# Performance work log

Measured on AMD Instinct MI355X. Metric: run time of the kernel, lower is better.

The kernel has to match this reference:

```python
import jax, jax.numpy as jnp
import numpy as np
from jax import lax

N = 1_000_000
H = 1024
POOL = 8
NF = 16
NS = 50
K = 5
PAD = (K - 1) // 2
D_IN = 3 + NF + NS  # 69
EPS = 1e-4


def setup_inputs() -> dict:
    key = jax.random.key(0)
    ks = jax.random.split(key, 14)
    def dense(k, fan_in, fan_out):
        lim = 1.0 / np.sqrt(fan_in)
        kw, kb = jax.random.split(k)
        w = jax.random.uniform(kw, (fan_in, fan_out), jnp.float32, -lim, lim)
        b = jax.random.uniform(kb, (fan_out,), jnp.float32, -lim, lim)
        return w, b
    x = jax.random.uniform(ks[0], (N, 2), jnp.float32)
    s = jax.random.normal(ks[1], (N, 1), jnp.float32)
    sse = jax.random.normal(ks[2], (N, NS), jnp.float32)
    sdf = jax.random.normal(ks[3], (1, 2, H, H), jnp.float32)
    lim_c = 1.0 / np.sqrt(2 * K * K)
    conv_w = jax.random.uniform(ks[4], (NF, 2, K, K), jnp.float32, -lim_c, lim_c)
    conv_b = jax.random.uniform(ks[5], (NF,), jnp.float32, -lim_c, lim_c)
    w1, b1 = dense(ks[6], D_IN, 128)
    w2, b2 = dense(ks[7], 128, 128)
    w3, b3 = dense(ks[8], 128, 96)
    w4, b4 = dense(ks[9], 96, 1)
    return {"x": x, "s": s, "sse": sse, "sdf": sdf,
            "conv_w": conv_w, "conv_b": conv_b,
            "w1": w1, "b1": b1, "w2": w2, "b2": b2,
            "w3": w3, "b3": b3, "w4": w4, "b4": b4}


def tensor_interp2d(A, pts, dx):
    # A: [C, Hh, Ww] feature map; pts: [N, 2] coords in [0,1] -> returns [N, C]
    C, Hh, Ww = A.shape
    gx = jnp.clip(pts[:, 0], dx, 1.0 - dx) * (Ww - 1)
    gy = jnp.clip(pts[:, 1], dx, 1.0 - dx) * (Hh - 1)
    x0 = jnp.floor(gx).astype(jnp.int32)
    y0 = jnp.floor(gy).astype(jnp.int32)
    x1 = jnp.minimum(x0 + 1, Ww - 1)
    y1 = jnp.minimum(y0 + 1, Hh - 1)
    wx = (gx - x0)[None, :]  # [1, N]
    wy = (gy - y0)[None, :]
    f00 = A[:, y0, x0]  # [C, N]
    f10 = A[:, y0, x1]
    f01 = A[:, y1, x0]
    f11 = A[:, y1, x1]
    out = (f00 * (1 - wx) * (1 - wy) + f10 * wx * (1 - wy)
           + f01 * (1 - wx) * wy + f11 * wx * wy)
    return out.T  # [N, C]


def reference(x, s, sse, sdf, conv_w, conv_b, w1, b1, w2, b2, w3, b3, w4, b4):
    # AvgPool2d(8, stride=8): exact reshape-mean since stride == kernel
    B, Cin, Hh, Ww = sdf.shape
    pooled = sdf.reshape(B, Cin, Hh // POOL, POOL, Ww // POOL, POOL).mean(axis=(3, 5))
    feat = lax.conv_general_dilated(pooled, conv_w, (1, 1), [(PAD, PAD), (PAD, PAD)],
                                    dimension_numbers=("NCHW", "OIHW", "NCHW"))
    feat = feat + conv_b[None, :, None, None]
    A = feat[0]  # squeeze -> [NF, 128, 128]
    x1 = tensor_interp2d(A, x, EPS)  # [N, NF]
    h = jnp.concatenate((x, s, sse, x1), axis=1)  # [N, 69]
    h = jax.nn.relu(h @ w1 + b1)
    h = jax.nn.relu(h @ w2 + b2)
    h = jax.nn.relu(h @ w3 + b3)
    return h @ w4 + b4  # [N, 1]
```

## Files before the change

kernel.cpp:

```cpp
#include <hip/hip_runtime.h>

#define EPS_ 1e-4f

typedef _Float16 f16;
typedef _Float16 f16x8 __attribute__((ext_vector_type(8)));
typedef _Float16 f16x4 __attribute__((ext_vector_type(4)));
typedef _Float16 f16x2 __attribute__((ext_vector_type(2)));
typedef __fp16 h16x2 __attribute__((ext_vector_type(2)));
typedef float f32x4v __attribute__((ext_vector_type(4)));
typedef float f32x2v __attribute__((ext_vector_type(2)));
typedef unsigned int u32;

__device__ inline f32x4v mfma16(f16x8 a, f16x8 b, f32x4v c) {
    return __builtin_amdgcn_mfma_f32_16x16x32_f16(a, b, c, 0, 0, 0);
}
__device__ inline f16x2 pk2(float a, float b) {
    h16x2 r = __builtin_amdgcn_cvt_pkrtz(a, b);
    return __builtin_bit_cast(f16x2, r);
}
__device__ inline u32 bc32(f16x2 v) { return __builtin_bit_cast(u32, v); }

__device__ inline f16x8 zero8() {
    f16x8 r;
#pragma unroll
    for (int i = 0; i < 8; i++) r[i] = (f16)0.f;
    return r;
}

__device__ inline f16x8 cvt8x2(f32x2v a, f32x2v b, f32x2v c, f32x2v d) {
    f16x2 p0 = pk2(a.x, a.y), p1 = pk2(b.x, b.y), p2 = pk2(c.x, c.y), p3 = pk2(d.x, d.y);
    f16x8 r;
    r[0] = p0[0]; r[1] = p0[1]; r[2] = p1[0]; r[3] = p1[1];
    r[4] = p2[0]; r[5] = p2[1]; r[6] = p3[0]; r[7] = p3[1];
    return r;
}

__global__ void pool_kernel(const float* __restrict__ sdf, float* __restrict__ pooled) {
    int t = blockIdx.x * blockDim.x + threadIdx.x;
    int c = t >> 14;
    int rem = t & 16383;
    int R = rem >> 7;
    int C = rem & 127;
    const float* base = sdf + c * 1048576 + (R * 8) * 1024 + C * 8;
    float sum = 0.f;
#pragma unroll
    for (int r = 0; r < 8; r++) {
        const float4* p = (const float4*)(base + r * 1024);
        float4 a = p[0];
        float4 b = p[1];
        sum += a.x + a.y + a.z + a.w + b.x + b.y + b.z + b.w;
    }
    pooled[t] = sum * (1.f / 64.f);
}

__global__ void conv_kernel(const float* __restrict__ pooled,
                            const float* __restrict__ conv_w,
                            const float* __restrict__ conv_b,
                            float* __restrict__ A) {
    int t = blockIdx.x * blockDim.x + threadIdx.x;
    int y = t >> 7, x = t & 127;
    float acc[16];
#pragma unroll
    for (int f = 0; f < 16; f++) acc[f] = conv_b[f];
#pragma unroll
    for (int c = 0; c < 2; c++) {
#pragma unroll
        for (int ky = 0; ky < 5; ky++) {
            int yy = y + ky - 2;
            if (yy < 0 || yy > 127) continue;
#pragma unroll
            for (int kx = 0; kx < 5; kx++) {
                int xx = x + kx - 2;
                if (xx < 0 || xx > 127) continue;
                float v = pooled[c * 16384 + yy * 128 + xx];
                int wbase = c * 25 + ky * 5 + kx;
#pragma unroll
                for (int f = 0; f < 16; f++)
                    acc[f] = fmaf(v, conv_w[f * 50 + wbase], acc[f]);
            }
        }
    }
    float4* out4 = (float4*)(A + t * 16);
#pragma unroll
    for (int q = 0; q < 4; q++)
        out4[q] = make_float4(acc[4 * q], acc[4 * q + 1], acc[4 * q + 2], acc[4 * q + 3]);
}

__global__ void pack_kernel(const float* __restrict__ w1, const float* __restrict__ b1,
                            const float* __restrict__ w2, const float* __restrict__ w3,
                            f16* __restrict__ frags) {
    int t = blockIdx.x * blockDim.x + threadIdx.x;
    if (t >= 80 * 64) return;
    int f = t >> 6, lane = t & 63;
    int g = lane >> 4, col = lane & 15;
    f16 v[8];
    if (f < 24) {
        int mf = f / 3, kc = f % 3;
        int o = mf * 16 + col;
#pragma unroll
        for (int i = 0; i < 8; i++) {
            int k = kc * 32 + g * 8 + i;
            float val = 0.f;
            if (k < 50) val = w1[(3 + k) * 128 + o];
            else if (k == 50) val = w1[0 * 128 + o];
            else if (k == 51) val = w1[1 * 128 + o];
            else if (k == 52) val = w1[2 * 128 + o];
            else if (k >= 56 && k < 72) val = w1[(53 + (k - 56)) * 128 + o];
            else if (k == 72) val = b1[o];
            v[i] = (f16)val;
        }
    } else if (f < 56) {
        int ff = f - 24, mf = ff >> 2, kc = ff & 3;
        int o = mf * 16 + col;
#pragma unroll
        for (int i = 0; i < 8; i++) {
            int k = kc * 32 + g * 8 + i;
            v[i] = (f16)w2[k * 128 + o];
        }
    } else {
        int ff = f - 56, mf = ff >> 2, kc = ff & 3;
        int o = mf * 16 + col;
#pragma unroll
        for (int i = 0; i < 8; i++) {
            int k = kc * 32 + g * 8 + i;
            v[i] = (f16)w3[k * 96 + o];
        }
    }
    f16* dst = frags + (f * 64 + lane) * 8;
#pragma unroll
    for (int i = 0; i < 8; i++) dst[i] = v[i];
}

__global__ void __launch_bounds__(768, 3) mlp_kernel(
    const float* __restrict__ x, const float* __restrict__ s,
    const float* __restrict__ sse, const float* __restrict__ Amat,
    const float4* __restrict__ fragsv,
    const float* __restrict__ b2, const float* __restrict__ b3,
    const float* __restrict__ w4, const float* __restrict__ b4,
    float* __restrict__ out) {
    __shared__ f16 wlds[40960];
    __shared__ f16 acth[12][2048];
    __shared__ float bias2[128];
    __shared__ float bias3[96];
    __shared__ float w4l[96];

    const int tid = threadIdx.x;
    const int wv = tid >> 6;
    const int lane = tid & 63;
    const int g = lane >> 4, col = lane & 15;
    const int swz = (col & 7) << 3;

    {
        float4* wl4 = (float4*)wlds;
        for (int i = tid; i < 5120; i += 768) wl4[i] = fragsv[i];
        if (tid < 128) bias2[tid] = b2[tid];
        if (tid < 96) { bias3[tid] = b3[tid]; w4l[tid] = w4[tid]; }
    }
    __syncthreads();
    const float b4v = b4[0];

    f16* ah = acth[wv];
    u32* ibA = (u32*)ah;
    u32* ibB = (u32*)ah + 192;

    const int wtotal = 31250;
    int wg = blockIdx.x * 12 + wv;
    const int wstride = gridDim.x * 12;

    f32x2v Axv, Bxv;

    auto INTERP = [&](f32x2v xv, u32* ib) {
        float gx = fminf(fmaxf(xv.x, EPS_), 1.f - EPS_) * 127.f;
        float gy = fminf(fmaxf(xv.y, EPS_), 1.f - EPS_) * 127.f;
        float fx0 = floorf(gx), fy0 = floorf(gy);
        int ix0 = (int)fx0, iy0 = (int)fy0;
        int ix1 = min(ix0 + 1, 127), iy1 = min(iy0 + 1, 127);
        float wx = gx - fx0, wy = gy - fy0;
        const f32x4v* A4 = (const f32x4v*)Amat;
        f32x4v f00 = A4[(iy0 * 128 + ix0) * 4 + g];
        f32x4v f10 = A4[(iy0 * 128 + ix1) * 4 + g];
        f32x4v f01 = A4[(iy1 * 128 + ix0) * 4 + g];
        f32x4v f11 = A4[(iy1 * 128 + ix1) * 4 + g];
        float w00 = (1.f - wx) * (1.f - wy), w10 = wx * (1.f - wy);
        float w01 = (1.f - wx) * wy, w11 = wx * wy;
        f32x4v r = f00 * w00 + f10 * w10 + f01 * w01 + f11 * w11;
        uint2 uv;
        uv.x = bc32(pk2(r.x, r.y));
        uv.y = bc32(pk2(r.z, r.w));
        *(uint2*)(ib + col * 12 + 2 * g) = uv;
    };

    auto LOADBUILD = [&](int pt0, f32x2v xv, const u32* ib, f16x8* bf) {
        const float* base = sse + (long)(pt0 + col) * 50;
        f32x2v c0[4];
#pragma unroll
        for (int q = 0; q < 4; q++) c0[q] = *(const f32x2v*)(base + 8 * g + 2 * q);
        bf[0] = cvt8x2(c0[0], c0[1], c0[2], c0[3]);
        if (g < 2) {
            f32x2v c1[4];
#pragma unroll
            for (int q = 0; q < 4; q++) c1[q] = *(const f32x2v*)(base + 32 + 8 * g + 2 * q);
            bf[1] = cvt8x2(c1[0], c1[1], c1[2], c1[3]);
        } else if (g == 2) {
            f32x2v e = *(const f32x2v*)(base + 48);
            float sv = s[pt0 + col];
            f16x8 t = zero8();
            t[0] = (f16)e.x; t[1] = (f16)e.y;
            t[2] = (f16)xv.x; t[3] = (f16)xv.y;
            t[4] = (f16)sv;
            bf[1] = t;
        } else {
            bf[1] = *(const f16x8*)(ib + col * 12);
        }
        if (g == 0) {
            bf[2] = *(const f16x8*)(ib + col * 12 + 4);
        } else if (g == 1) {
            f16x8 t = zero8();
            t[0] = (f16)1.f;
            bf[2] = t;
        } else {
            bf[2] = zero8();
        }
    };

    auto TRANS = [&](f32x4v* acc, const float* bias, f16x8* hbf) {
#pragma unroll
        for (int mf = 0; mf < 8; mf++) {
            f32x4v v = acc[mf];
            if (bias) {
                f32x4v bb = *(const f32x4v*)&bias[mf * 16 + g * 4];
                v = v + bb;
            }
            uint2 uv;
            uv.x = bc32(pk2(fmaxf(v.x, 0.f), fmaxf(v.y, 0.f)));
            uv.y = bc32(pk2(fmaxf(v.z, 0.f), fmaxf(v.w, 0.f)));
            *(uint2*)&ah[(col * 128 + mf * 16 + g * 4) ^ swz] = uv;
        }
#pragma unroll
        for (int kc = 0; kc < 4; kc++)
            hbf[kc] = *(const f16x8*)&ah[(col * 128 + kc * 32 + g * 8) ^ swz];
    };

    auto L4OUT = [&](f32x4v* acc3, int pt0) {
        float partial = 0.f;
#pragma unroll
        for (int mf = 0; mf < 6; mf++) {
            f32x4v bb = *(const f32x4v*)&bias3[mf * 16 + g * 4];
            f32x4v wv4 = *(const f32x4v*)&w4l[mf * 16 + g * 4];
            partial += fmaxf(acc3[mf].x + bb.x, 0.f) * wv4.x;
            partial += fmaxf(acc3[mf].y + bb.y, 0.f) * wv4.y;
            partial += fmaxf(acc3[mf].z + bb.z, 0.f) * wv4.z;
            partial += fmaxf(acc3[mf].w + bb.w, 0.f) * wv4.w;
        }
        partial += __shfl_xor(partial, 16);
        partial += __shfl_xor(partial, 32);
        if (g == 0) out[pt0 + col] = partial + b4v;
    };

    if (wg < wtotal) {
        Axv = *(const f32x2v*)(x + 2 * (wg * 32 + col));
        Bxv = *(const f32x2v*)(x + 2 * (wg * 32 + 16 + col));
    }

    for (; wg < wtotal; wg += wstride) {
        const int pt0 = wg * 32;

        INTERP(Axv, ibA);
        INTERP(Bxv, ibB);

        f16x8 bfA[3], bfB[3];
        LOADBUILD(pt0, Axv, ibA, bfA);
        LOADBUILD(pt0 + 16, Bxv, ibB, bfB);

        int wgn = wg + wstride;
        if (wgn < wtotal) {
            Axv = *(const f32x2v*)(x + 2 * (wgn * 32 + col));
            Bxv = *(const f32x2v*)(x + 2 * (wgn * 32 + 16 + col));
        }

        f32x4v accA[8], accB[8];
#pragma unroll
        for (int mf = 0; mf < 8; mf++) {
            accA[mf] = (f32x4v)(0.f);
            accB[mf] = (f32x4v)(0.f);
        }
#pragma unroll
        for (int kc = 0; kc < 3; kc++) {
#pragma unroll
            for (int mf = 0; mf < 8; mf++) {
                f16x8 wf = *(const f16x8*)&wlds[((mf * 3 + kc) * 64 + lane) * 8];
                accA[mf] = mfma16(wf, bfA[kc], accA[mf]);
                accB[mf] = mfma16(wf, bfB[kc], accB[mf]);
            }
        }

        f16x8 hbfA[4], hbfB[4];
        TRANS(accA, nullptr, hbfA);
        TRANS(accB, nullptr, hbfB);

        f32x4v acc2A[8], acc2B[8];
#pragma unroll
        for (int mf = 0; mf < 8; mf++) {
            acc2A[mf] = (f32x4v)(0.f);
            acc2B[mf] = (f32x4v)(0.f);
        }
#pragma unroll
        for (int kc = 0; kc < 4; kc++) {
#pragma unroll
            for (int mf = 0; mf < 8; mf++) {
                f16x8 wf = *(const f16x8*)&wlds[((24 + mf * 4 + kc) * 64 + lane) * 8];
                acc2A[mf] = mfma16(wf, hbfA[kc], acc2A[mf]);
                acc2B[mf] = mfma16(wf, hbfB[kc], acc2B[mf]);
            }
        }

        TRANS(acc2A, bias2, hbfA);
        TRANS(acc2B, bias2, hbfB);

        f32x4v acc3A[6], acc3B[6];
#pragma unroll
        for (int mf = 0; mf < 6; mf++) {
            acc3A[mf] = (f32x4v)(0.f);
            acc3B[mf] = (f32x4v)(0.f);
        }
#pragma unroll
        for (int kc = 0; kc < 4; kc++) {
#pragma unroll
            for (int mf = 0; mf < 6; mf++) {
                f16x8 wf = *(const f16x8*)&wlds[((56 + mf * 4 + kc) * 64 + lane) * 8];
                acc3A[mf] = mfma16(wf, hbfA[kc], acc3A[mf]);
                acc3B[mf] = mfma16(wf, hbfB[kc], acc3B[mf]);
            }
        }

        L4OUT(acc3A, pt0);
        L4OUT(acc3B, pt0 + 16);
    }
}

extern "C" void kernel_launch(void* const* d_in, const int* in_sizes, int n_in,
                              void* d_out, int out_size, void* d_ws, size_t ws_size,
                              hipStream_t stream) {
    const float* x      = (const float*)d_in[0];
    const float* s      = (const float*)d_in[1];
    const float* sse    = (const float*)d_in[2];
    const float* sdf    = (const float*)d_in[3];
    const float* conv_w = (const float*)d_in[4];
    const float* conv_b = (const float*)d_in[5];
    const float* w1     = (const float*)d_in[6];
    const float* b1     = (const float*)d_in[7];
    const float* w2     = (const float*)d_in[8];
    const float* b2     = (const float*)d_in[9];
    const float* w3     = (const float*)d_in[10];
    const float* b3     = (const float*)d_in[11];
    const float* w4     = (const float*)d_in[12];
    const float* b4     = (const float*)d_in[13];
    float* out = (float*)d_out;

    float* pooled = (float*)d_ws;
    float* A      = pooled + 32768;
    f16*   frags  = (f16*)d_ws;

    pool_kernel<<<128, 256, 0, stream>>>(sdf, pooled);
    conv_kernel<<<64, 256, 0, stream>>>(pooled, conv_w, conv_b, A);
    pack_kernel<<<20, 256, 0, stream>>>(w1, b1, w2, w3, frags);
    mlp_kernel<<<256, 768, 0, stream>>>(x, s, sse, A, (const float4*)frags,
                                        b2, b3, w4, b4, out);
}
```

Measured before the change: 135.7 us.

## Software-pipeline next tile's sse/x loads and interpolation across MLP layers

Restructures the persistent MLP loop so global loads for the next 32-point tile (sse, s, x) are issued before the current tile's layer-1 MFMAs, then converted and interpolated piecemeal between later layers. The aim is to hide global memory latency behind matrix work. It also drops the min-blocks-per-CU launch bound so the compiler can use more registers, which raises register pressure and may lower occupancy.

```diff
diff --git a/kernel.cpp b/kernel.cpp
--- a/kernel.cpp
+++ b/kernel.cpp
@@ -4,7 +4,6 @@
 
 typedef _Float16 f16;
 typedef _Float16 f16x8 __attribute__((ext_vector_type(8)));
-typedef _Float16 f16x4 __attribute__((ext_vector_type(4)));
 typedef _Float16 f16x2 __attribute__((ext_vector_type(2)));
 typedef __fp16 h16x2 __attribute__((ext_vector_type(2)));
 typedef float f32x4v __attribute__((ext_vector_type(4)));
@@ -33,6 +32,14 @@
     r[0] = p0[0]; r[1] = p0[1]; r[2] = p1[0]; r[3] = p1[1];
     r[4] = p2[0]; r[5] = p2[1]; r[6] = p3[0]; r[7] = p3[1];
     return r;
+}
+
+__device__ inline f16x8 mkg2(f32x2v e, f32x2v xv, float sv) {
+    f16x8 t = zero8();
+    t[0] = (f16)e.x; t[1] = (f16)e.y;
+    t[2] = (f16)xv.x; t[3] = (f16)xv.y;
+    t[4] = (f16)sv;
+    return t;
 }
 
 __global__ void pool_kernel(const float* __restrict__ sdf, float* __restrict__ pooled) {
@@ -131,7 +138,7 @@
     for (int i = 0; i < 8; i++) dst[i] = v[i];
 }
 
-__global__ void __launch_bounds__(768, 3) mlp_kernel(
+__global__ void __launch_bounds__(768) mlp_kernel(
     const float* __restrict__ x, const float* __restrict__ s,
     const float* __restrict__ sse, const float* __restrict__ Amat,
     const float4* __restrict__ fragsv,
@@ -167,7 +174,27 @@
     int wg = blockIdx.x * 12 + wv;
     const int wstride = gridDim.x * 12;
 
-    f32x2v Axv, Bxv;
+    f32x2v Ac0[4], Ac1[4], Ae, Axv; float Asv;
+    f32x2v Bc0[4], Bc1[4], Be, Bxv; float Bsv;
+    f16x8 bfA[3], bfB[3];
+
+    auto ISSUE0 = [&](int pt0, f32x2v* c0, f32x2v& e, f32x2v& xv, float& sv) {
+        const float* base = sse + (long)(pt0 + col) * 50;
+#pragma unroll
+        for (int q = 0; q < 4; q++) c0[q] = *(const f32x2v*)(base + 8 * g + 2 * q);
+        if (g == 2) {
+            e = *(const f32x2v*)(base + 48);
+            sv = s[pt0 + col];
+        }
+        xv = *(const f32x2v*)(x + 2 * (pt0 + col));
+    };
+    auto ISSUE1 = [&](int pt0, f32x2v* c1) {
+        if (g < 2) {
+            const float* base = sse + (long)(pt0 + col) * 50;
+#pragma unroll
+            for (int q = 0; q < 4; q++) c1[q] = *(const f32x2v*)(base + 32 + 8 * g + 2 * q);
+        }
+    };
 
     auto INTERP = [&](f32x2v xv, u32* ib) {
         float gx = fminf(fmaxf(xv.x, EPS_), 1.f - EPS_) * 127.f;
@@ -190,39 +217,6 @@
         *(uint2*)(ib + col * 12 + 2 * g) = uv;
     };
 
-    auto LOADBUILD = [&](int pt0, f32x2v xv, const u32* ib, f16x8* bf) {
-        const float* base = sse + (long)(pt0 + col) * 50;
-        f32x2v c0[4];
-#pragma unroll
-        for (int q = 0; q < 4; q++) c0[q] = *(const f32x2v*)(base + 8 * g + 2 * q);
-        bf[0] = cvt8x2(c0[0], c0[1], c0[2], c0[3]);
-        if (g < 2) {
-            f32x2v c1[4];
-#pragma unroll
-            for (int q = 0; q < 4; q++) c1[q] = *(const f32x2v*)(base + 32 + 8 * g + 2 * q);
-            bf[1] = cvt8x2(c1[0], c1[1], c1[2], c1[3]);
-        } else if (g == 2) {
-            f32x2v e = *(const f32x2v*)(base + 48);
-            float sv = s[pt0 + col];
-            f16x8 t = zero8();
-            t[0] = (f16)e.x; t[1] = (f16)e.y;
-            t[2] = (f16)xv.x; t[3] = (f16)xv.y;
-            t[4] = (f16)sv;
-            bf[1] = t;
-        } else {
-            bf[1] = *(const f16x8*)(ib + col * 12);
-        }
-        if (g == 0) {
-            bf[2] = *(const f16x8*)(ib + col * 12 + 4);
-        } else if (g == 1) {
-            f16x8 t = zero8();
-            t[0] = (f16)1.f;
-            bf[2] = t;
-        } else {
-            bf[2] = zero8();
-        }
-    };
-
     auto TRANS = [&](f32x4v* acc, const float* bias, f16x8* hbf) {
 #pragma unroll
         for (int mf = 0; mf < 8; mf++) {
@@ -258,24 +252,44 @@
     };
 
     if (wg < wtotal) {
-        Axv = *(const f32x2v*)(x + 2 * (wg * 32 + col));
-        Bxv = *(const f32x2v*)(x + 2 * (wg * 32 + 16 + col));
+        ISSUE0(wg * 32, Ac0, Ae, Axv, Asv);
+        ISSUE0(wg * 32 + 16, Bc0, Be, Bxv, Bsv);
+        ISSUE1(wg * 32, Ac1);
+        ISSUE1(wg * 32 + 16, Bc1);
+        INTERP(Axv, ibA);
+        INTERP(Bxv, ibB);
+        bfA[0] = cvt8x2(Ac0[0], Ac0[1], Ac0[2], Ac0[3]);
+        bfB[0] = cvt8x2(Bc0[0], Bc0[1], Bc0[2], Bc0[3]);
+        if (g < 2) {
+            bfA[1] = cvt8x2(Ac1[0], Ac1[1], Ac1[2], Ac1[3]);
+            bfB[1] = cvt8x2(Bc1[0], Bc1[1], Bc1[2], Bc1[3]);
+        } else if (g == 2) {
+            bfA[1] = mkg2(Ae, Axv, Asv);
+            bfB[1] = mkg2(Be, Bxv, Bsv);
+        } else {
+            bfA[1] = *(const f16x8*)(ibA + col * 12);
+            bfB[1] = *(const f16x8*)(ibB + col * 12);
+        }
+        if (g == 0) {
+            bfA[2] = *(const f16x8*)(ibA + col * 12 + 4);
+            bfB[2] = *(const f16x8*)(ibB + col * 12 + 4);
+        } else if (g == 1) {
+            f16x8 t = zero8();
+            t[0] = (f16)1.f;
+            bfA[2] = t; bfB[2] = t;
+        } else {
+            bfA[2] = zero8(); bfB[2] = zero8();
+        }
     }
 
     for (; wg < wtotal; wg += wstride) {
         const int pt0 = wg * 32;
-
-        INTERP(Axv, ibA);
-        INTERP(Bxv, ibB);
-
-        f16x8 bfA[3], bfB[3];
-        LOADBUILD(pt0, Axv, ibA, bfA);
-        LOADBUILD(pt0 + 16, Bxv, ibB, bfB);
-
-        int wgn = wg + wstride;
-        if (wgn < wtotal) {
-            Axv = *(const f32x2v*)(x + 2 * (wgn * 32 + col));
-            Bxv = *(const f32x2v*)(x + 2 * (wgn * 32 + 16 + col));
+        const int wgn = wg + wstride;
+        const bool more = (wgn < wtotal);
+
+        if (more) {
+            ISSUE0(wgn * 32, Ac0, Ae, Axv, Asv);
+            ISSUE0(wgn * 32 + 16, Bc0, Be, Bxv, Bsv);
         }
 
         f32x4v accA[8], accB[8];
@@ -294,6 +308,17 @@
             }
         }
 
+        if (more) {
+            bfA[0] = cvt8x2(Ac0[0], Ac0[1], Ac0[2], Ac0[3]);
+            bfB[0] = cvt8x2(Bc0[0], Bc0[1], Bc0[2], Bc0[3]);
+            if (g == 2) {
+                bfA[1] = mkg2(Ae, Axv, Asv);
+                bfB[1] = mkg2(Be, Bxv, Bsv);
+            }
+            ISSUE1(wgn * 32, Ac1);
+            ISSUE1(wgn * 32 + 16, Bc1);
+        }
+
         f16x8 hbfA[4], hbfB[4];
         TRANS(accA, nullptr, hbfA);
         TRANS(accB, nullptr, hbfB);
@@ -314,8 +339,18 @@
             }
         }
 
+        if (more && g < 2) {
+            bfA[1] = cvt8x2(Ac1[0], Ac1[1], Ac1[2], Ac1[3]);
+            bfB[1] = cvt8x2(Bc1[0], Bc1[1], Bc1[2], Bc1[3]);
+        }
+
         TRANS(acc2A, bias2, hbfA);
         TRANS(acc2B, bias2, hbfB);
+
+        if (more) {
+            INTERP(Axv, ibA);
+            INTERP(Bxv, ibB);
+        }
 
         f32x4v acc3A[6], acc3B[6];
 #pragma unroll
@@ -330,6 +365,17 @@
                 f16x8 wf = *(const f16x8*)&wlds[((56 + mf * 4 + kc) * 64 + lane) * 8];
                 acc3A[mf] = mfma16(wf, hbfA[kc], acc3A[mf]);
                 acc3B[mf] = mfma16(wf, hbfB[kc], acc3B[mf]);
+            }
+        }
+
+        if (more) {
+            if (g == 3) {
+                bfA[1] = *(const f16x8*)(ibA + col * 12);
+                bfB[1] = *(const f16x8*)(ibB + col * 12);
+            }
+            if (g == 0) {
+                bfA[2] = *(const f16x8*)(ibA + col * 12 + 4);
+                bfB[2] = *(const f16x8*)(ibB + col * 12 + 4);
             }
         }
 
```

After: 196.5 us. 1.45x slower.
